# Performance work log

Hardware: AMD Instinct MI355X
Metric: run time of the kernel (lower is better)

The kernel has to match this reference:

```python
import jax, jax.numpy as jnp
import numpy as np

# Dimensions (source globals scaled to production: r=256 residues, s=128 sequences)
S, R, CM, CZ, C, H = 128, 256, 256, 128, 32, 8
EPS = 1e-5  # torch LayerNorm default


def setup_inputs() -> dict:
    key = jax.random.key(0)
    ks = jax.random.split(key, 14)
    msa = jax.random.normal(ks[0], (S, R, CM), dtype=jnp.float32)
    pair = jax.random.normal(ks[1], (R, R, CZ), dtype=jnp.float32)
    u = lambda k, shape, fan: jax.random.uniform(k, shape, jnp.float32, -1.0 / np.sqrt(fan), 1.0 / np.sqrt(fan))
    return {
        "msa": msa,
        "pair": pair,
        # per-head LayerNorm affine params (stacked over head axis)
        "ln_msa_g": 1.0 + 0.1 * jax.random.normal(ks[2], (H, CM), dtype=jnp.float32),
        "ln_msa_b": 0.1 * jax.random.normal(ks[3], (H, CM), dtype=jnp.float32),
        "ln_pair_g": 1.0 + 0.1 * jax.random.normal(ks[4], (H, CZ), dtype=jnp.float32),
        "ln_pair_b": 0.1 * jax.random.normal(ks[5], (H, CZ), dtype=jnp.float32),
        # per-head projections (torch Linear without bias; stored as (in, out))
        "Wq": u(ks[6], (H, CM, C), CM),
        "Wk": u(ks[7], (H, CM, C), CM),
        "Wv": u(ks[8], (H, CM, C), CM),
        "Wg": u(ks[9], (H, CM, C), CM),
        "Wb": u(ks[10], (H, CZ, S), CZ),  # linear_b: c_z -> s
        # output projection c*H -> c_m (with bias)
        "Wo": u(ks[11], (H * C, CM), H * C),
        "bo": u(ks[12], (CM,), H * C),
    }


def _forward(msa, pair, ln_msa_g, ln_msa_b, ln_pair_g, ln_pair_b, Wq, Wk, Wv, Wg, Wb, Wo, bo):
    # LayerNorm normalization is head-independent; only affine differs per head.
    mu = msa.mean(-1, keepdims=True)
    var = msa.var(-1, keepdims=True)
    nm = (msa - mu) * jax.lax.rsqrt(var + EPS)              # (S, R, CM)
    p = nm[None] * ln_msa_g[:, None, None, :] + ln_msa_b[:, None, None, :]  # (H, S, R, CM)

    q = jnp.einsum("hsrc,hcd->hsrd", p, Wq)                  # (H, S, R, C)
    k = jnp.einsum("hsrc,hcd->hsrd", p, Wk)
    v = jnp.einsum("hsrc,hcd->hsrd", p, Wv)
    g = jax.nn.sigmoid(jnp.einsum("hsrc,hcd->hsrd", p, Wg))

    pmu = pair.mean(-1, keepdims=True)
    pvar = pair.var(-1, keepdims=True)
    npair = (pair - pmu) * jax.lax.rsqrt(pvar + EPS)         # (R, R, CZ)
    pp = npair[None] * ln_pair_g[:, None, None, :] + ln_pair_b[:, None, None, :]  # (H, R, R, CZ)
    bflat = jnp.einsum("hijc,hcs->hijs", pp, Wb)             # (H, R, R, S)
    # Faithful to torch: b = linear_b(flat_pair).view(s, r, r) -- a raw
    # row-major reinterpretation (NOT a transpose).
    b = bflat.reshape(H, S, R, R)

    inv_sqrt_c = np.float32(1.0 / np.sqrt(C))
    scores = (jnp.einsum("hsid,hsjd->hsij", q, k) + b) * inv_sqrt_c  # (H, S, R, R)
    # Source softmax is over dim=-2 (the query/row axis), faithful here.
    a = jax.nn.softmax(scores, axis=-2)
    o = g * jnp.einsum("hsij,hsjd->hsid", a, v)              # (H, S, R, C)

    # concat heads on last dim: (S, R, H*C)
    cat = jnp.transpose(o, (1, 2, 0, 3)).reshape(S, R, H * C)
    return cat @ Wo + bo                                      # (S, R, CM)


def reference(msa, pair, ln_msa_g, ln_msa_b, ln_pair_g, ln_pair_b, Wq, Wk, Wv, Wg, Wb, Wo, bo):
    return _forward(msa, pair, ln_msa_g, ln_msa_b, ln_pair_g, ln_pair_b, Wq, Wk, Wv, Wg, Wb, Wo, bo)
```

## Files before the change

### kernel.cpp

```cpp
#include <hip/hip_runtime.h>
#include <hip/hip_bf16.h>


namespace {
constexpr int S_ = 128, R_ = 256, CM_ = 256, CZ_ = 128, C_ = 32, H_ = 8;
constexpr int SR_ = S_ * R_;
constexpr int RR_ = R_ * R_;
constexpr float EPS_ = 1e-5f;
constexpr float ISC_ = 0.17677669529663687f;

constexpr size_t OFF_MU_M = 0;
constexpr size_t OFF_RS_M = OFF_MU_M + SR_;
constexpr size_t OFF_WC   = OFF_RS_M + SR_;
constexpr size_t OFF_BC   = OFF_WC + (size_t)H_ * CM_ * 128;
constexpr size_t OFF_WBP  = OFF_BC + (size_t)H_ * 128;
constexpr size_t OFF_BBP  = OFF_WBP + (size_t)H_ * CZ_ * 128;
constexpr size_t F32_END  = OFF_BBP + (size_t)H_ * 128;
constexpr size_t BF_BASE  = F32_END * 4;
constexpr size_t QKVG_ELEMS = (size_t)H_ * SR_ * C_;
constexpr size_t CAT_ELEMS  = (size_t)SR_ * CM_;
constexpr size_t WBT_ELEMS  = (size_t)H_ * 128 * 128;
constexpr size_t WOT_ELEMS  = (size_t)256 * 256;
constexpr size_t PAIRN_ELEMS = (size_t)RR_ * 128;
constexpr size_t NEED_BYTES =
    BF_BASE + (4 * QKVG_ELEMS + CAT_ELEMS + WBT_ELEMS + WOT_ELEMS + PAIRN_ELEMS) * 2;
}

typedef unsigned short bf_t;
typedef short s8v __attribute__((ext_vector_type(8)));
typedef float f4v __attribute__((ext_vector_type(4)));

__device__ __forceinline__ unsigned pk2(float lo, float hi) {
  __hip_bfloat162 t = __float22bfloat162_rn(float2{lo, hi});
  return *reinterpret_cast<unsigned*>(&t);
}
__device__ __forceinline__ bf_t pk1(float v) {
  __hip_bfloat16 t = __float2bfloat16(v);
  return *reinterpret_cast<bf_t*>(&t);
}
__device__ __forceinline__ float uplo(unsigned u) { return __uint_as_float(u << 16); }
__device__ __forceinline__ float uphi(unsigned u) { return __uint_as_float(u & 0xffff0000u); }
__device__ __forceinline__ f4v mfma16(s8v a, s8v b, f4v c) {
  return __builtin_amdgcn_mfma_f32_16x16x32_bf16(a, b, c, 0, 0, 0);
}
__device__ __forceinline__ s8v ld8(const bf_t* p) { return *reinterpret_cast<const s8v*>(p); }

__global__ void msa_stats_k(const float* __restrict__ msa, float* __restrict__ mu,
                            float* __restrict__ rstd) {
  int row = blockIdx.x * 4 + (threadIdx.x >> 6);
  int lane = threadIdx.x & 63;
  float4 v = reinterpret_cast<const float4*>(msa + (size_t)row * CM_)[lane];
  float s = v.x + v.y + v.z + v.w;
  float s2 = v.x * v.x + v.y * v.y + v.z * v.z + v.w * v.w;
  for (int off = 32; off; off >>= 1) {
    s += __shfl_down(s, off);
    s2 += __shfl_down(s2, off);
  }
  if (lane == 0) {
    float m = s / CM_;
    float var = s2 / CM_ - m * m;
    mu[row] = m;
    rstd[row] = rsqrtf(var + EPS_);
  }
}

__global__ __launch_bounds__(512) void pair_norm_k(const float* __restrict__ pair,
                                                   bf_t* __restrict__ pairN) {
  int row = blockIdx.x * 8 + (threadIdx.x >> 6);
  int lane = threadIdx.x & 63;
  float2 v = reinterpret_cast<const float2*>(pair + (size_t)row * CZ_)[lane];
  float s = v.x + v.y;
  float s2 = v.x * v.x + v.y * v.y;
  for (int off = 32; off; off >>= 1) {
    s += __shfl_xor(s, off);
    s2 += __shfl_xor(s2, off);
  }
  float m = s / CZ_;
  float var = s2 / CZ_ - m * m;
  float rs = rsqrtf(var + EPS_);
  reinterpret_cast<unsigned*>(pairN)[(size_t)row * 64 + lane] =
      pk2((v.x - m) * rs, (v.y - m) * rs);
}

__global__ void prep_small_k(const float* __restrict__ lnb_m, const float* __restrict__ lnb_p,
                             const float* __restrict__ Wq, const float* __restrict__ Wk,
                             const float* __restrict__ Wv, const float* __restrict__ Wg,
                             const float* __restrict__ Wb, float* __restrict__ bc,
                             float* __restrict__ bbp) {
  int b = blockIdx.x;
  int t = threadIdx.x;
  if (b < H_) {
    int h = b;
    int m = t >> 5, d = t & 31;
    const float* Wsrc = (m == 0) ? Wq : (m == 1) ? Wk : (m == 2) ? Wv : Wg;
    float scale = (m == 0) ? ISC_ : 1.0f;
    float bias = 0.f;
    for (int c = 0; c < CM_; c++) bias += lnb_m[h * CM_ + c] * Wsrc[((size_t)h * CM_ + c) * C_ + d];
    bc[h * 128 + t] = bias * scale;
  } else {
    int h = b - H_;
    float bias = 0.f;
    for (int c = 0; c < CZ_; c++) bias += lnb_p[h * CZ_ + c] * Wb[((size_t)h * CZ_ + c) * S_ + t];
    bbp[h * 128 + t] = bias * ISC_;
  }
}

__global__ __launch_bounds__(256) void prep_wide_k(
    const float* __restrict__ lng_m, const float* __restrict__ lng_p,
    const float* __restrict__ Wq, const float* __restrict__ Wk, const float* __restrict__ Wv,
    const float* __restrict__ Wg, const float* __restrict__ Wb, const float* __restrict__ Wo,
    bf_t* __restrict__ wct, bf_t* __restrict__ wbt, bf_t* __restrict__ wot) {
  int idx = blockIdx.x * 256 + threadIdx.x;
  if (idx < 262144) {
    int h = idx >> 15, rem = idx & 32767;
    int j = rem >> 8, c = rem & 255;
    int m = j >> 5, d = j & 31;
    const float* Wsrc = (m == 0) ? Wq : (m == 1) ? Wk : (m == 2) ? Wv : Wg;
    float scale = (m == 0) ? ISC_ : 1.0f;
    wct[idx] = pk1(lng_m[h * CM_ + c] * Wsrc[((size_t)h * CM_ + c) * C_ + d] * scale);
  } else if (idx < 262144 + 131072) {
    int i2 = idx - 262144;
    int h = i2 >> 14, rem = i2 & 16383;
    int t = rem >> 7, c = rem & 127;
    wbt[i2] = pk1(lng_p[h * CZ_ + c] * Wb[((size_t)h * CZ_ + c) * S_ + t] * ISC_);
  } else {
    int i3 = idx - 262144 - 131072;
    int n = i3 >> 8, k = i3 & 255;
    wot[i3] = pk1(Wo[(size_t)k * 256 + n]);
  }
}

__global__ __launch_bounds__(512, 1) void qkvg_mfma_k(
    const float* __restrict__ msa, const float* __restrict__ mu, const float* __restrict__ rstd,
    const bf_t* __restrict__ wct, const float* __restrict__ bc, bf_t* __restrict__ q,
    bf_t* __restrict__ k, bf_t* __restrict__ v, bf_t* __restrict__ g) {
  __shared__ bf_t sm_a[128 * 256];
  __shared__ bf_t sm_w[128 * 256];
  int ib = blockIdx.x;
  int tid = threadIdx.x;
  int w = tid >> 6, l = tid & 63;
  int l15 = l & 15, l4 = l >> 4;
  int iw = w >> 2, jw = w & 3;
  int sr0 = ib * 128;
  int sx7 = l15 & 7;
#pragma unroll
  for (int rep = 0; rep < 8; rep++) {
    int flat = rep * 512 + tid;
    int row = flat >> 5, c = flat & 31;
    int srow = sr0 + row;
    const float4* ps = reinterpret_cast<const float4*>(msa + (size_t)srow * CM_ + c * 8);
    float4 x0 = ps[0], x1 = ps[1];
    float m = mu[srow], rs = rstd[srow];
    uint4 wv;
    wv.x = pk2((x0.x - m) * rs, (x0.y - m) * rs);
    wv.y = pk2((x0.z - m) * rs, (x0.w - m) * rs);
    wv.z = pk2((x1.x - m) * rs, (x1.y - m) * rs);
    wv.w = pk2((x1.z - m) * rs, (x1.w - m) * rs);
    *reinterpret_cast<uint4*>(&sm_a[row * 256 + ((c ^ (row & 7)) << 3)]) = wv;
  }
  for (int h = 0; h < H_; h++) {
    __syncthreads();
#pragma unroll
    for (int rep = 0; rep < 8; rep++) {
      int flat = rep * 512 + tid;
      int row = flat >> 5, c = flat & 31;
      *reinterpret_cast<uint4*>(&sm_w[row * 256 + ((c ^ (row & 7)) << 3)]) =
          *reinterpret_cast<const uint4*>(wct + ((size_t)h * 128 + row) * 256 + c * 8);
    }
    f4v acc[4][2];
#pragma unroll
    for (int jt = 0; jt < 2; jt++) {
      float bb = bc[h * 128 + jw * 32 + jt * 16 + l15];
#pragma unroll
      for (int it = 0; it < 4; it++) acc[it][jt] = f4v{bb, bb, bb, bb};
    }
    __syncthreads();
#pragma unroll
    for (int ks = 0; ks < 8; ks++) {
      int ch = ks * 4 + l4;
      s8v a[4], b[2];
#pragma unroll
      for (int it = 0; it < 4; it++)
        a[it] = ld8(&sm_a[(iw * 64 + it * 16 + l15) * 256 + ((ch ^ sx7) << 3)]);
#pragma unroll
      for (int jt = 0; jt < 2; jt++)
        b[jt] = ld8(&sm_w[(jw * 32 + jt * 16 + l15) * 256 + ((ch ^ sx7) << 3)]);
#pragma unroll
      for (int it = 0; it < 4; it++)
#pragma unroll
        for (int jt = 0; jt < 2; jt++) acc[it][jt] = mfma16(a[it], b[jt], acc[it][jt]);
    }
#pragma unroll
    for (int it = 0; it < 4; it++) {
#pragma unroll
      for (int jt = 0; jt < 2; jt++) {
        int j = jw * 32 + jt * 16 + l15;
        int m_ = j >> 5, d = j & 31;
        bf_t* dst = (m_ == 0) ? q : (m_ == 1) ? k : (m_ == 2) ? v : g;
#pragma unroll
        for (int r = 0; r < 4; r++) {
          int i = iw * 64 + it * 16 + l4 * 4 + r;
          float val = acc[it][jt][r];
          if (m_ == 3) val = 1.f / (1.f + __expf(-val));
          dst[((size_t)h * SR_ + sr0 + i) * C_ + d] = pk1(val);
        }
      }
    }
  }
}

__global__ __launch_bounds__(512, 1) void attn_mfma_k(
    const bf_t* __restrict__ pairN, const bf_t* __restrict__ wbt,
    const float* __restrict__ bbp, const bf_t* __restrict__ qg, const bf_t* __restrict__ kg,
    const bf_t* __restrict__ vg, const bf_t* __restrict__ gg, bf_t* __restrict__ cat) {
  __shared__ bf_t sm_pN[256 * 128];
  __shared__ bf_t sm_wt[64 * 128];
  __shared__ bf_t sm_p[256 * 64];
  __shared__ bf_t sm_q[256 * 40];
  __shared__ bf_t sm_k[64 * 40];
  __shared__ bf_t sm_vt[32 * 64];
  __shared__ float sm_redm[4 * 64];
  __shared__ float sm_reds[4 * 64];

  int s = blockIdx.x, h = blockIdx.y;
  int tid = threadIdx.x;
  int w = tid >> 6, l = tid & 63;
  int l15 = l & 15, l4 = l >> 4;
  int iw = w >> 1, jw = w & 1;
  int iw2 = w >> 1, dw = w & 1;
  size_t base = ((size_t)h * SR_ + (size_t)s * R_) * C_;

#pragma unroll
  for (int rep = 0; rep < 2; rep++) {
    int flat = rep * 512 + tid;
    int row = flat >> 2, c = flat & 3;
    *reinterpret_cast<uint4*>(&sm_q[row * 40 + c * 8]) =
        *reinterpret_cast<const uint4*>(qg + base + (size_t)row * C_ + c * 8);
  }

  f4v accO[4];
#pragma unroll
  for (int it = 0; it < 4; it++) accO[it] = f4v{0.f, 0.f, 0.f, 0.f};

  for (int p = 0; p < 2; p++) {
    __syncthreads();
#pragma unroll
    for (int rep = 0; rep < 8; rep++) {
      int flat = rep * 512 + tid;
      int row = flat >> 4, c = flat & 15;
      int gr = (2 * s + (row >> 7)) * 256 + 2 * (row & 127) + p;
      *reinterpret_cast<uint4*>(&sm_pN[row * 128 + ((c ^ (row & 7)) << 3)]) =
          *reinterpret_cast<const uint4*>(pairN + (size_t)gr * 128 + c * 8);
    }
    for (int jh = 0; jh < 2; jh++) {
      int j0 = p * 128 + jh * 64;
      __syncthreads();
#pragma unroll
      for (int rep = 0; rep < 2; rep++) {
        int flat = rep * 512 + tid;
        int row = flat >> 4, c = flat & 15;
        *reinterpret_cast<uint4*>(&sm_wt[row * 128 + ((c ^ (row & 7)) << 3)]) =
            *reinterpret_cast<const uint4*>(wbt + ((size_t)h * 128 + jh * 64 + row) * 128 +
                                            c * 8);
      }
      if (tid < 256) {
        int row = tid >> 2, c = tid & 3;
        *reinterpret_cast<uint4*>(&sm_k[row * 40 + c * 8]) =
            *reinterpret_cast<const uint4*>(kg + base + (size_t)(j0 + row) * C_ + c * 8);
      } else {
        int t2 = tid - 256;
        int j = t2 >> 2, dc = t2 & 3;
        uint4 u = *reinterpret_cast<const uint4*>(vg + base + (size_t)(j0 + j) * C_ + dc * 8);
        unsigned uu[4] = {u.x, u.y, u.z, u.w};
#pragma unroll
        for (int e = 0; e < 8; e++) {
          int d = dc * 8 + e;
          bf_t val = (bf_t)((uu[e >> 1] >> ((e & 1) * 16)) & 0xffff);
          sm_vt[d * 64 + ((((j >> 3) ^ (d & 7)) << 3) + (j & 7))] = val;
        }
      }
      f4v acc[4][2];
      {
        float bb0 = bbp[h * 128 + jh * 64 + jw * 32 + l15];
        float bb1 = bbp[h * 128 + jh * 64 + jw * 32 + 16 + l15];
#pragma unroll
        for (int it = 0; it < 4; it++) {
          acc[it][0] = f4v{bb0, bb0, bb0, bb0};
          acc[it][1] = f4v{bb1, bb1, bb1, bb1};
        }
      }
      __syncthreads();
      int sx7 = l15 & 7;
#pragma unroll
      for (int ks = 0; ks < 4; ks++) {
        int ch = (ks * 4 + l4);
        s8v a[4], b[2];
#pragma unroll
        for (int it = 0; it < 4; it++)
          a[it] = ld8(&sm_pN[(iw * 64 + it * 16 + l15) * 128 + ((ch ^ sx7) << 3)]);
#pragma unroll
        for (int u = 0; u < 2; u++)
          b[u] = ld8(&sm_wt[(jw * 32 + u * 16 + l15) * 128 + ((ch ^ sx7) << 3)]);
#pragma unroll
        for (int it = 0; it < 4; it++) {
          acc[it][0] = mfma16(a[it], b[0], acc[it][0]);
          acc[it][1] = mfma16(a[it], b[1], acc[it][1]);
        }
      }
      {
        s8v qa[4], kb[2];
#pragma unroll
        for (int it = 0; it < 4; it++)
          qa[it] = ld8(&sm_q[(iw * 64 + it * 16 + l15) * 40 + l4 * 8]);
#pragma unroll
        for (int u = 0; u < 2; u++)
          kb[u] = ld8(&sm_k[(jw * 32 + u * 16 + l15) * 40 + l4 * 8]);
#pragma unroll
        for (int it = 0; it < 4; it++) {
          acc[it][0] = mfma16(qa[it], kb[0], acc[it][0]);
          acc[it][1] = mfma16(qa[it], kb[1], acc[it][1]);
        }
      }
      float mx[2];
#pragma unroll
      for (int u = 0; u < 2; u++) {
        float m0 = -1e30f;
#pragma unroll
        for (int it = 0; it < 4; it++)
#pragma unroll
          for (int r = 0; r < 4; r++) m0 = fmaxf(m0, acc[it][u][r]);
        m0 = fmaxf(m0, __shfl_xor(m0, 16));
        m0 = fmaxf(m0, __shfl_xor(m0, 32));
        mx[u] = m0;
      }
      if (l < 16) {
        sm_redm[iw * 64 + jw * 32 + l] = mx[0];
        sm_redm[iw * 64 + jw * 32 + 16 + l] = mx[1];
      }
      __syncthreads();
      float M[2], sm[2];
#pragma unroll
      for (int u = 0; u < 2; u++) {
        int jc = jw * 32 + u * 16 + l15;
        float m0 = sm_redm[jc];
        m0 = fmaxf(m0, sm_redm[64 + jc]);
        m0 = fmaxf(m0, sm_redm[128 + jc]);
        m0 = fmaxf(m0, sm_redm[192 + jc]);
        M[u] = m0;
        float s0 = 0.f;
#pragma unroll
        for (int it = 0; it < 4; it++) {
#pragma unroll
          for (int r = 0; r < 4; r++) {
            float e = __expf(acc[it][u][r] - m0);
            acc[it][u][r] = e;
            s0 += e;
          }
        }
        s0 += __shfl_xor(s0, 16);
        s0 += __shfl_xor(s0, 32);
        sm[u] = s0;
      }
      if (l < 16) {
        sm_reds[iw * 64 + jw * 32 + l] = sm[0];
        sm_reds[iw * 64 + jw * 32 + 16 + l] = sm[1];
      }
      __syncthreads();
#pragma unroll
      for (int u = 0; u < 2; u++) {
        int jc = jw * 32 + u * 16 + l15;
        float tot = sm_reds[jc] + sm_reds[64 + jc] + sm_reds[128 + jc] + sm_reds[192 + jc];
        float inv = 1.0f / tot;
#pragma unroll
        for (int it = 0; it < 4; it++) {
#pragma unroll
          for (int r = 0; r < 4; r++) {
            int i = iw * 64 + it * 16 + l4 * 4 + r;
            sm_p[i * 64 + ((((jc >> 3) ^ (i & 7)) << 3) + (jc & 7))] = pk1(acc[it][u][r] * inv);
          }
        }
      }
      __syncthreads();
#pragma unroll
      for (int ks = 0; ks < 2; ks++) {
        int ch = ks * 4 + l4;
        s8v vb = ld8(&sm_vt[(dw * 16 + l15) * 64 + ((ch ^ sx7) << 3)]);
#pragma unroll
        for (int it = 0; it < 4; it++) {
          s8v pa = ld8(&sm_p[(iw2 * 64 + it * 16 + l15) * 64 + ((ch ^ sx7) << 3)]);
          accO[it] = mfma16(pa, vb, accO[it]);
        }
      }
    }
  }
#pragma unroll
  for (int it = 0; it < 4; it++) {
#pragma unroll
    for (int r = 0; r < 4; r++) {
      int i = iw2 * 64 + it * 16 + l4 * 4 + r;
      int d = dw * 16 + l15;
      float gf = uplo((unsigned)gg[base + (size_t)i * C_ + d]);
      cat[((size_t)s * R_ + i) * 256 + h * 32 + d] = pk1(accO[it][r] * gf);
    }
  }
}

__global__ __launch_bounds__(512, 1) void out_mfma_k(const bf_t* __restrict__ cat,
                                                     const bf_t* __restrict__ wot,
                                                     const float* __restrict__ bo,
                                                     float* __restrict__ out) {
  __shared__ bf_t sm_a[128 * 256];
  __shared__ bf_t sm_b[128 * 256];
  int ib = blockIdx.x;
  int tid = threadIdx.x;
  int w = tid >> 6, l = tid & 63;
  int l15 = l & 15, l4 = l >> 4, sx7 = l15 & 7;
  int iw = w >> 2, jw = w & 3;
  int sr0 = ib * 128;
#pragma unroll
  for (int rep = 0; rep < 8; rep++) {
    int flat = rep * 512 + tid;
    int row = flat >> 5, c = flat & 31;
    *reinterpret_cast<uint4*>(&sm_a[row * 256 + ((c ^ (row & 7)) << 3)]) =
        *reinterpret_cast<const uint4*>(cat + (size_t)(sr0 + row) * 256 + c * 8);
  }
  for (int nb = 0; nb < 2; nb++) {
    __syncthreads();
#pragma unroll
    for (int rep = 0; rep < 8; rep++) {
      int flat = rep * 512 + tid;
      int row = flat >> 5, c = flat & 31;
      *reinterpret_cast<uint4*>(&sm_b[row * 256 + ((c ^ (row & 7)) << 3)]) =
          *reinterpret_cast<const uint4*>(wot + (size_t)(nb * 128 + row) * 256 + c * 8);
    }
    f4v acc[4][2];
#pragma unroll
    for (int jt = 0; jt < 2; jt++) {
      float bb = bo[nb * 128 + jw * 32 + jt * 16 + l15];
#pragma unroll
      for (int it = 0; it < 4; it++) acc[it][jt] = f4v{bb, bb, bb, bb};
    }
    __syncthreads();
#pragma unroll
    for (int ks = 0; ks < 8; ks++) {
      int ch = ks * 4 + l4;
      s8v a[4], b[2];
#pragma unroll
      for (int it = 0; it < 4; it++)
        a[it] = ld8(&sm_a[(iw * 64 + it * 16 + l15) * 256 + ((ch ^ sx7) << 3)]);
#pragma unroll
      for (int jt = 0; jt < 2; jt++)
        b[jt] = ld8(&sm_b[(jw * 32 + jt * 16 + l15) * 256 + ((ch ^ sx7) << 3)]);
#pragma unroll
      for (int it = 0; it < 4; it++)
#pragma unroll
        for (int jt = 0; jt < 2; jt++) acc[it][jt] = mfma16(a[it], b[jt], acc[it][jt]);
    }
#pragma unroll
    for (int it = 0; it < 4; it++)
#pragma unroll
      for (int jt = 0; jt < 2; jt++) {
        int n = nb * 128 + jw * 32 + jt * 16 + l15;
#pragma unroll
        for (int r = 0; r < 4; r++) {
          int i = iw * 64 + it * 16 + l4 * 4 + r;
          out[(size_t)(sr0 + i) * 256 + n] = acc[it][jt][r];
        }
      }
  }
}

extern "C" void kernel_launch(void* const* d_in, const int* in_sizes, int n_in, void* d_out,
                              int out_size, void* d_ws, size_t ws_size, hipStream_t stream) {
  if (ws_size < NEED_BYTES) return;

  const float* msa = (const float*)d_in[0];
  const float* pair = (const float*)d_in[1];
  const float* lng_m = (const float*)d_in[2];
  const float* lnb_m = (const float*)d_in[3];
  const float* lng_p = (const float*)d_in[4];
  const float* lnb_p = (const float*)d_in[5];
  const float* Wq = (const float*)d_in[6];
  const float* Wk = (const float*)d_in[7];
  const float* Wv = (const float*)d_in[8];
  const float* Wg = (const float*)d_in[9];
  const float* Wb = (const float*)d_in[10];
  const float* Wo = (const float*)d_in[11];
  const float* bo = (const float*)d_in[12];
  float* out = (float*)d_out;
  float* ws = (float*)d_ws;

  float* mu_m = ws + OFF_MU_M;
  float* rs_m = ws + OFF_RS_M;
  bf_t* wct = (bf_t*)(ws + OFF_WC);
  float* bc = ws + OFF_BC;
  float* bbp = ws + OFF_BBP;
  bf_t* qb = (bf_t*)((char*)d_ws + BF_BASE);
  bf_t* kb = qb + QKVG_ELEMS;
  bf_t* vb = kb + QKVG_ELEMS;
  bf_t* gb = vb + QKVG_ELEMS;
  bf_t* cat = gb + QKVG_ELEMS;
  bf_t* wbt = cat + CAT_ELEMS;
  bf_t* wot = wbt + WBT_ELEMS;
  bf_t* pairN = wot + WOT_ELEMS;

  msa_stats_k<<<SR_ / 4, 256, 0, stream>>>(msa, mu_m, rs_m);
  pair_norm_k<<<RR_ / 8, 512, 0, stream>>>(pair, pairN);
  prep_small_k<<<2 * H_, 128, 0, stream>>>(lnb_m, lnb_p, Wq, Wk, Wv, Wg, Wb, bc, bbp);
  prep_wide_k<<<1792, 256, 0, stream>>>(lng_m, lng_p, Wq, Wk, Wv, Wg, Wb, Wo, wct, wbt, wot);
  qkvg_mfma_k<<<SR_ / 128, 512, 0, stream>>>(msa, mu_m, rs_m, wct, bc, qb, kb, vb, gb);
  attn_mfma_k<<<dim3(S_, H_), 512, 0, stream>>>(pairN, wbt, bbp, qb, kb, vb, gb, cat);
  out_mfma_k<<<SR_ / 128, 512, 0, stream>>>(cat, wot, bo, out);
}
```

Before: 173.7 us.

## Merge norm kernels, precompute bf16 msa, merge softmax reductions, remap attention blocks

Combines the msa and pair LayerNorm passes into one launch that writes normalized msa as bf16, so the QKVG kernel loads bf16 directly instead of reading fp32 msa plus stats. The column softmax now computes a local max and sum in a single pass and combines them across warps with rescaling, removing one barrier and one shared-memory round trip. The attention grid becomes 1D with a swizzled block-to-(s,h) mapping, likely to improve cache locality for shared pair data across heads. This adds an extra bf16 msa buffer write and read in exchange.

```diff
diff --git a/kernel.cpp b/kernel.cpp
--- a/kernel.cpp
+++ b/kernel.cpp
@@ -9,21 +9,20 @@
 constexpr float EPS_ = 1e-5f;
 constexpr float ISC_ = 0.17677669529663687f;
 
-constexpr size_t OFF_MU_M = 0;
-constexpr size_t OFF_RS_M = OFF_MU_M + SR_;
-constexpr size_t OFF_WC   = OFF_RS_M + SR_;
-constexpr size_t OFF_BC   = OFF_WC + (size_t)H_ * CM_ * 128;
-constexpr size_t OFF_WBP  = OFF_BC + (size_t)H_ * 128;
-constexpr size_t OFF_BBP  = OFF_WBP + (size_t)H_ * CZ_ * 128;
-constexpr size_t F32_END  = OFF_BBP + (size_t)H_ * 128;
-constexpr size_t BF_BASE  = F32_END * 4;
-constexpr size_t QKVG_ELEMS = (size_t)H_ * SR_ * C_;
-constexpr size_t CAT_ELEMS  = (size_t)SR_ * CM_;
-constexpr size_t WBT_ELEMS  = (size_t)H_ * 128 * 128;
-constexpr size_t WOT_ELEMS  = (size_t)256 * 256;
+constexpr size_t OFF_WC  = 0;
+constexpr size_t OFF_BC  = 131072;
+constexpr size_t OFF_BBP = 132096;
+constexpr size_t F32_END = 133120;
+constexpr size_t BF_BASE = F32_END * 4;
+constexpr size_t QKVG_ELEMS  = (size_t)H_ * SR_ * C_;
+constexpr size_t CAT_ELEMS   = (size_t)SR_ * CM_;
+constexpr size_t WBT_ELEMS   = (size_t)H_ * 128 * 128;
+constexpr size_t WOT_ELEMS   = (size_t)256 * 256;
 constexpr size_t PAIRN_ELEMS = (size_t)RR_ * 128;
+constexpr size_t MSAN_ELEMS  = (size_t)SR_ * 256;
 constexpr size_t NEED_BYTES =
-    BF_BASE + (4 * QKVG_ELEMS + CAT_ELEMS + WBT_ELEMS + WOT_ELEMS + PAIRN_ELEMS) * 2;
+    BF_BASE +
+    (4 * QKVG_ELEMS + CAT_ELEMS + WBT_ELEMS + WOT_ELEMS + PAIRN_ELEMS + MSAN_ELEMS) * 2;
 }
 
 typedef unsigned short bf_t;
@@ -39,47 +38,46 @@
   return *reinterpret_cast<bf_t*>(&t);
 }
 __device__ __forceinline__ float uplo(unsigned u) { return __uint_as_float(u << 16); }
-__device__ __forceinline__ float uphi(unsigned u) { return __uint_as_float(u & 0xffff0000u); }
 __device__ __forceinline__ f4v mfma16(s8v a, s8v b, f4v c) {
   return __builtin_amdgcn_mfma_f32_16x16x32_bf16(a, b, c, 0, 0, 0);
 }
 __device__ __forceinline__ s8v ld8(const bf_t* p) { return *reinterpret_cast<const s8v*>(p); }
 
-__global__ void msa_stats_k(const float* __restrict__ msa, float* __restrict__ mu,
-                            float* __restrict__ rstd) {
-  int row = blockIdx.x * 4 + (threadIdx.x >> 6);
+__global__ __launch_bounds__(512) void norm_all_k(const float* __restrict__ pair,
+                                                  const float* __restrict__ msa,
+                                                  bf_t* __restrict__ pairN,
+                                                  bf_t* __restrict__ msaN) {
+  int b = blockIdx.x;
   int lane = threadIdx.x & 63;
-  float4 v = reinterpret_cast<const float4*>(msa + (size_t)row * CM_)[lane];
-  float s = v.x + v.y + v.z + v.w;
-  float s2 = v.x * v.x + v.y * v.y + v.z * v.z + v.w * v.w;
-  for (int off = 32; off; off >>= 1) {
-    s += __shfl_down(s, off);
-    s2 += __shfl_down(s2, off);
-  }
-  if (lane == 0) {
+  if (b < RR_ / 8) {
+    int row = b * 8 + (threadIdx.x >> 6);
+    float2 v = reinterpret_cast<const float2*>(pair + (size_t)row * CZ_)[lane];
+    float s = v.x + v.y;
+    float s2 = v.x * v.x + v.y * v.y;
+    for (int off = 32; off; off >>= 1) {
+      s += __shfl_xor(s, off);
+      s2 += __shfl_xor(s2, off);
+    }
+    float m = s / CZ_;
+    float rs = rsqrtf(s2 / CZ_ - m * m + EPS_);
+    reinterpret_cast<unsigned*>(pairN)[(size_t)row * 64 + lane] =
+        pk2((v.x - m) * rs, (v.y - m) * rs);
+  } else {
+    int row = (b - RR_ / 8) * 8 + (threadIdx.x >> 6);
+    float4 v = reinterpret_cast<const float4*>(msa + (size_t)row * CM_)[lane];
+    float s = v.x + v.y + v.z + v.w;
+    float s2 = v.x * v.x + v.y * v.y + v.z * v.z + v.w * v.w;
+    for (int off = 32; off; off >>= 1) {
+      s += __shfl_xor(s, off);
+      s2 += __shfl_xor(s2, off);
+    }
     float m = s / CM_;
-    float var = s2 / CM_ - m * m;
-    mu[row] = m;
-    rstd[row] = rsqrtf(var + EPS_);
-  }
-}
-
-__global__ __launch_bounds__(512) void pair_norm_k(const float* __restrict__ pair,
-                                                   bf_t* __restrict__ pairN) {
-  int row = blockIdx.x * 8 + (threadIdx.x >> 6);
-  int lane = threadIdx.x & 63;
-  float2 v = reinterpret_cast<const float2*>(pair + (size_t)row * CZ_)[lane];
-  float s = v.x + v.y;
-  float s2 = v.x * v.x + v.y * v.y;
-  for (int off = 32; off; off >>= 1) {
-    s += __shfl_xor(s, off);
-    s2 += __shfl_xor(s2, off);
-  }
-  float m = s / CZ_;
-  float var = s2 / CZ_ - m * m;
-  float rs = rsqrtf(var + EPS_);
-  reinterpret_cast<unsigned*>(pairN)[(size_t)row * 64 + lane] =
-      pk2((v.x - m) * rs, (v.y - m) * rs);
+    float rs = rsqrtf(s2 / CM_ - m * m + EPS_);
+    uint2 wv;
+    wv.x = pk2((v.x - m) * rs, (v.y - m) * rs);
+    wv.y = pk2((v.z - m) * rs, (v.w - m) * rs);
+    reinterpret_cast<uint2*>(msaN)[(size_t)row * 64 + lane] = wv;
+  }
 }
 
 __global__ void prep_small_k(const float* __restrict__ lnb_m, const float* __restrict__ lnb_p,
@@ -131,9 +129,8 @@
 }
 
 __global__ __launch_bounds__(512, 1) void qkvg_mfma_k(
-    const float* __restrict__ msa, const float* __restrict__ mu, const float* __restrict__ rstd,
-    const bf_t* __restrict__ wct, const float* __restrict__ bc, bf_t* __restrict__ q,
-    bf_t* __restrict__ k, bf_t* __restrict__ v, bf_t* __restrict__ g) {
+    const bf_t* __restrict__ msaN, const bf_t* __restrict__ wct, const float* __restrict__ bc,
+    bf_t* __restrict__ q, bf_t* __restrict__ k, bf_t* __restrict__ v, bf_t* __restrict__ g) {
   __shared__ bf_t sm_a[128 * 256];
   __shared__ bf_t sm_w[128 * 256];
   int ib = blockIdx.x;
@@ -147,16 +144,8 @@
   for (int rep = 0; rep < 8; rep++) {
     int flat = rep * 512 + tid;
     int row = flat >> 5, c = flat & 31;
-    int srow = sr0 + row;
-    const float4* ps = reinterpret_cast<const float4*>(msa + (size_t)srow * CM_ + c * 8);
-    float4 x0 = ps[0], x1 = ps[1];
-    float m = mu[srow], rs = rstd[srow];
-    uint4 wv;
-    wv.x = pk2((x0.x - m) * rs, (x0.y - m) * rs);
-    wv.y = pk2((x0.z - m) * rs, (x0.w - m) * rs);
-    wv.z = pk2((x1.x - m) * rs, (x1.y - m) * rs);
-    wv.w = pk2((x1.z - m) * rs, (x1.w - m) * rs);
-    *reinterpret_cast<uint4*>(&sm_a[row * 256 + ((c ^ (row & 7)) << 3)]) = wv;
+    *reinterpret_cast<uint4*>(&sm_a[row * 256 + ((c ^ (row & 7)) << 3)]) =
+        *reinterpret_cast<const uint4*>(msaN + (size_t)(sr0 + row) * 256 + c * 8);
   }
   for (int h = 0; h < H_; h++) {
     __syncthreads();
@@ -222,7 +211,12 @@
   __shared__ float sm_redm[4 * 64];
   __shared__ float sm_reds[4 * 64];
 
-  int s = blockIdx.x, h = blockIdx.y;
+  int b = blockIdx.x;
+  int x = b & 7, t = b >> 3;
+  int round = t >> 5, inner = t & 31;
+  int sl = inner >> 3, h = inner & 7;
+  int s = (round * 8 + x) * 4 + sl;
+
   int tid = threadIdx.x;
   int w = tid >> 6, l = tid & 63;
   int l15 = l & 15, l4 = l >> 4;
@@ -294,17 +288,17 @@
 #pragma unroll
       for (int ks = 0; ks < 4; ks++) {
         int ch = (ks * 4 + l4);
-        s8v a[4], b[2];
+        s8v a[4], b2[2];
 #pragma unroll
         for (int it = 0; it < 4; it++)
           a[it] = ld8(&sm_pN[(iw * 64 + it * 16 + l15) * 128 + ((ch ^ sx7) << 3)]);
 #pragma unroll
         for (int u = 0; u < 2; u++)
-          b[u] = ld8(&sm_wt[(jw * 32 + u * 16 + l15) * 128 + ((ch ^ sx7) << 3)]);
+          b2[u] = ld8(&sm_wt[(jw * 32 + u * 16 + l15) * 128 + ((ch ^ sx7) << 3)]);
 #pragma unroll
         for (int it = 0; it < 4; it++) {
-          acc[it][0] = mfma16(a[it], b[0], acc[it][0]);
-          acc[it][1] = mfma16(a[it], b[1], acc[it][1]);
+          acc[it][0] = mfma16(a[it], b2[0], acc[it][0]);
+          acc[it][1] = mfma16(a[it], b2[1], acc[it][1]);
         }
       }
       {
@@ -321,7 +315,7 @@
           acc[it][1] = mfma16(qa[it], kb[1], acc[it][1]);
         }
       }
-      float mx[2];
+      float fac[2], mloc[2];
 #pragma unroll
       for (int u = 0; u < 2; u++) {
         float m0 = -1e30f;
@@ -331,54 +325,42 @@
           for (int r = 0; r < 4; r++) m0 = fmaxf(m0, acc[it][u][r]);
         m0 = fmaxf(m0, __shfl_xor(m0, 16));
         m0 = fmaxf(m0, __shfl_xor(m0, 32));
-        mx[u] = m0;
-      }
-      if (l < 16) {
-        sm_redm[iw * 64 + jw * 32 + l] = mx[0];
-        sm_redm[iw * 64 + jw * 32 + 16 + l] = mx[1];
-      }
-      __syncthreads();
-      float M[2], sm[2];
-#pragma unroll
-      for (int u = 0; u < 2; u++) {
-        int jc = jw * 32 + u * 16 + l15;
-        float m0 = sm_redm[jc];
-        m0 = fmaxf(m0, sm_redm[64 + jc]);
-        m0 = fmaxf(m0, sm_redm[128 + jc]);
-        m0 = fmaxf(m0, sm_redm[192 + jc]);
-        M[u] = m0;
         float s0 = 0.f;
 #pragma unroll
-        for (int it = 0; it < 4; it++) {
+        for (int it = 0; it < 4; it++)
 #pragma unroll
           for (int r = 0; r < 4; r++) {
             float e = __expf(acc[it][u][r] - m0);
             acc[it][u][r] = e;
             s0 += e;
           }
-        }
         s0 += __shfl_xor(s0, 16);
         s0 += __shfl_xor(s0, 32);
-        sm[u] = s0;
-      }
-      if (l < 16) {
-        sm_reds[iw * 64 + jw * 32 + l] = sm[0];
-        sm_reds[iw * 64 + jw * 32 + 16 + l] = sm[1];
+        mloc[u] = m0;
+        if (l < 16) {
+          sm_redm[iw * 64 + jw * 32 + u * 16 + l] = m0;
+          sm_reds[iw * 64 + jw * 32 + u * 16 + l] = s0;
+        }
       }
       __syncthreads();
 #pragma unroll
       for (int u = 0; u < 2; u++) {
         int jc = jw * 32 + u * 16 + l15;
-        float tot = sm_reds[jc] + sm_reds[64 + jc] + sm_reds[128 + jc] + sm_reds[192 + jc];
-        float inv = 1.0f / tot;
-#pragma unroll
-        for (int it = 0; it < 4; it++) {
+        float M = fmaxf(fmaxf(sm_redm[jc], sm_redm[64 + jc]),
+                        fmaxf(sm_redm[128 + jc], sm_redm[192 + jc]));
+        float tot = 0.f;
+#pragma unroll
+        for (int gx = 0; gx < 4; gx++)
+          tot += sm_reds[gx * 64 + jc] * __expf(sm_redm[gx * 64 + jc] - M);
+        fac[u] = __expf(mloc[u] - M) / tot;
+#pragma unroll
+        for (int it = 0; it < 4; it++)
 #pragma unroll
           for (int r = 0; r < 4; r++) {
             int i = iw * 64 + it * 16 + l4 * 4 + r;
-            sm_p[i * 64 + ((((jc >> 3) ^ (i & 7)) << 3) + (jc & 7))] = pk1(acc[it][u][r] * inv);
+            sm_p[i * 64 + ((((jc >> 3) ^ (i & 7)) << 3) + (jc & 7))] =
+                pk1(acc[it][u][r] * fac[u]);
           }
-        }
       }
       __syncthreads();
 #pragma unroll
@@ -490,8 +472,6 @@
   float* out = (float*)d_out;
   float* ws = (float*)d_ws;
 
-  float* mu_m = ws + OFF_MU_M;
-  float* rs_m = ws + OFF_RS_M;
   bf_t* wct = (bf_t*)(ws + OFF_WC);
   float* bc = ws + OFF_BC;
   float* bbp = ws + OFF_BBP;
@@ -503,12 +483,12 @@
   bf_t* wbt = cat + CAT_ELEMS;
   bf_t* wot = wbt + WBT_ELEMS;
   bf_t* pairN = wot + WOT_ELEMS;
-
-  msa_stats_k<<<SR_ / 4, 256, 0, stream>>>(msa, mu_m, rs_m);
-  pair_norm_k<<<RR_ / 8, 512, 0, stream>>>(pair, pairN);
+  bf_t* msaN = pairN + PAIRN_ELEMS;
+
+  norm_all_k<<<RR_ / 8 + SR_ / 8, 512, 0, stream>>>(pair, msa, pairN, msaN);
   prep_small_k<<<2 * H_, 128, 0, stream>>>(lnb_m, lnb_p, Wq, Wk, Wv, Wg, Wb, bc, bbp);
   prep_wide_k<<<1792, 256, 0, stream>>>(lng_m, lng_p, Wq, Wk, Wv, Wg, Wb, Wo, wct, wbt, wot);
-  qkvg_mfma_k<<<SR_ / 128, 512, 0, stream>>>(msa, mu_m, rs_m, wct, bc, qb, kb, vb, gb);
-  attn_mfma_k<<<dim3(S_, H_), 512, 0, stream>>>(pairN, wbt, bbp, qb, kb, vb, gb, cat);
+  qkvg_mfma_k<<<SR_ / 128, 512, 0, stream>>>(msaN, wct, bc, qb, kb, vb, gb);
+  attn_mfma_k<<<S_ * H_, 512, 0, stream>>>(pairN, wbt, bbp, qb, kb, vb, gb, cat);
   out_mfma_k<<<SR_ / 128, 512, 0, stream>>>(cat, wot, bo, out);
 }
```

Measured after the change: 168.1 us. 3.2% less time.
